# Kernel optimization log

Hardware: AMD Instinct MI355X
Metric: run time of the kernel (lower is better)

## Reference

```python
import jax, jax.numpy as jnp
import numpy as np

N = 100000   # nodes
E = 1600000  # edges
D = 128      # in_dim
H = 128      # hidden


def setup_inputs() -> dict:
    key = jax.random.key(0)
    k = jax.random.split(key, 6)
    x = jax.random.normal(k[0], (N, D), dtype=jnp.float32)
    edge_index = jax.random.randint(k[1], (2, E), 0, N, dtype=jnp.int64)
    s1 = 1.0 / np.sqrt(D)
    s2 = 1.0 / np.sqrt(H)
    W1 = jax.random.uniform(k[2], (D, H), jnp.float32, -s1, s1)
    b1 = jax.random.uniform(k[3], (H,), jnp.float32, -s1, s1)
    W2 = jax.random.uniform(k[4], (H, H), jnp.float32, -s2, s2)
    b2 = jax.random.uniform(k[5], (H,), jnp.float32, -s2, s2)
    return {"x": x, "W1": W1, "b1": b1, "W2": W2, "b2": b2,
            "edge_index": edge_index}


def reference(x, W1, b1, W2, b2, edge_index):
    n = x.shape[0]
    loop = jnp.arange(n, dtype=edge_index.dtype)
    src = jnp.concatenate([edge_index[0], loop])  # sources incl. self-loops
    dst = jnp.concatenate([edge_index[1], loop])  # targets incl. self-loops
    # symmetric GCN normalization: D^-1/2 A_hat D^-1/2
    deg = jax.ops.segment_sum(jnp.ones_like(dst, jnp.float32), dst,
                              num_segments=n)
    dinv = jnp.where(deg > 0, deg ** -0.5, 0.0)
    norm = dinv[src] * dinv[dst]  # [E+N]

    def gcn_conv(h, W, b):
        m = h @ W                                   # [N, H] transform first
        agg = jax.ops.segment_sum(norm[:, None] * m[src], dst,
                                  num_segments=n)   # gather-scale-scatter
        return agg + b

    h = jax.nn.relu(gcn_conv(x, W1, b1))  # dropout is identity in eval mode
    return gcn_conv(h, W2, b2)
```

## Files before the change

kernel.cpp:

```cpp
#include <hip/hip_runtime.h>


#define RB    9
#define RANGE 512
#define CAPB  16384
#define CHUNK 8192

typedef __attribute__((ext_vector_type(8))) short bf16x8;
typedef __attribute__((ext_vector_type(4))) float f32x4;

__device__ inline float bf_lo(unsigned w) { return __uint_as_float(w << 16); }
__device__ inline float bf_hi(unsigned w) { return __uint_as_float(w & 0xffff0000u); }
__device__ inline unsigned bf16pair(float lo, float hi) {
    unsigned a = __float_as_uint(lo), b = __float_as_uint(hi);
    a += 0x7fffu + ((a >> 16) & 1u);
    b += 0x7fffu + ((b >> 16) & 1u);
    return (a >> 16) | (b & 0xffff0000u);
}
__device__ inline unsigned short bf16rne(float f) {
    unsigned u = __float_as_uint(f);
    u += 0x7fffu + ((u >> 16) & 1u);
    return (unsigned short)(u >> 16);
}
__device__ inline float bf2f(unsigned short h) { return __uint_as_float(((unsigned)h) << 16); }

__global__ void detect_i64(const unsigned* ei, int E, int* flag) {
    __shared__ int nz;
    if (threadIdx.x == 0) nz = 0;
    __syncthreads();
    int samples = E < 2048 ? E : 2048;
    int cnt = 0;
    for (int i = threadIdx.x; i < samples; i += blockDim.x)
        if (ei[2 * i + 1] != 0u) cnt++;
    if (cnt) atomicAdd(&nz, cnt);
    __syncthreads();
    if (threadIdx.x == 0) *flag = (nz == 0) ? 1 : 0;
}

__global__ void init_gcur(unsigned* gcur, int NB) {
    int b = blockIdx.x * blockDim.x + threadIdx.x;
    if (b < NB) gcur[b] = (unsigned)b * CAPB;
}

__global__ __launch_bounds__(256) void bucketA(const unsigned* __restrict__ ei, int E, int n,
                                               const int* __restrict__ flag,
                                               unsigned* __restrict__ gcur,
                                               unsigned* __restrict__ recs) {
    __shared__ unsigned hist[512];
    __shared__ unsigned offs[512];
    const int t = threadIdx.x;
    const int NB = (n + RANGE - 1) >> RB;
    for (int i = t; i < NB; i += 256) hist[i] = 0u;
    __syncthreads();
    const int base = blockIdx.x * CHUNK;
    const bool i64 = (*flag != 0);
    unsigned rec[32], bk[32];
#pragma unroll
    for (int j = 0; j < 32; j++) {
        int i = base + j * 256 + t;
        unsigned bv = 0xffffffffu, rv = 0u;
        if (i < E) {
            unsigned s, d;
            if (i64) { s = ei[2 * (size_t)i]; d = ei[2 * ((size_t)E + i)]; }
            else     { s = ei[i];             d = ei[(size_t)E + i]; }
            bv = d >> RB;
            rv = (s << RB) | (d & (RANGE - 1));
            atomicAdd(&hist[bv], 1u);
        }
        rec[j] = rv; bk[j] = bv;
    }
    __syncthreads();
    for (int b = t; b < NB; b += 256) {
        unsigned h = hist[b];
        offs[b] = h ? atomicAdd(&gcur[b], h) : 0u;
    }
    __syncthreads();
#pragma unroll
    for (int j = 0; j < 32; j++) {
        unsigned b = bk[j];
        if (b != 0xffffffffu) {
            unsigned pos = atomicAdd(&offs[b], 1u);
            if (pos < (b + 1u) * CAPB) recs[pos] = rec[j];
        }
    }
}

__global__ __launch_bounds__(256) void bucket_deg(const unsigned* __restrict__ gcur,
                                                  const unsigned* __restrict__ recs,
                                                  unsigned* __restrict__ deg, int n) {
    __shared__ unsigned dl[RANGE];
    const int b = blockIdx.x, t = threadIdx.x;
    const int node0 = b << RB;
    for (int v = t; v < RANGE; v += 256) dl[v] = 1u;
    __syncthreads();
    unsigned base = (unsigned)b * CAPB;
    unsigned cnt = gcur[b] - base; if (cnt > CAPB) cnt = CAPB;
    for (unsigned i = t; i < cnt; i += 256)
        atomicAdd(&dl[recs[base + i] & (RANGE - 1)], 1u);
    __syncthreads();
    for (int v = t; v < RANGE; v += 256)
        if (node0 + v < n) deg[node0 + v] = dl[v];
}

__global__ void dinv_kernel(const unsigned* deg, float* dinv, int n) {
    int i = blockIdx.x * blockDim.x + threadIdx.x;
    if (i < n) dinv[i] = rsqrtf((float)deg[i]);
}

__global__ void scan_block_sums(const unsigned* deg, unsigned* partials, int n) {
    __shared__ unsigned sdata[256];
    int b = blockIdx.x, t = threadIdx.x;
    int base = b * 1024;
    unsigned s = 0;
    for (int j = 0; j < 4; j++) {
        int i = base + t * 4 + j;
        if (i < n) s += deg[i];
    }
    sdata[t] = s;
    __syncthreads();
    for (int stride = 128; stride > 0; stride >>= 1) {
        if (t < stride) sdata[t] += sdata[t + stride];
        __syncthreads();
    }
    if (t == 0) partials[b] = sdata[0];
}

__global__ void scan_partials(unsigned* partials, int nb) {
    if (threadIdx.x == 0 && blockIdx.x == 0) {
        unsigned run = 0;
        for (int i = 0; i < nb; i++) { unsigned v = partials[i]; partials[i] = run; run += v; }
    }
}

__global__ void scan_write(const unsigned* deg, const unsigned* partials,
                           int* row_off, int n) {
    int b = blockIdx.x, t = threadIdx.x;
    int lane = t & 63, wid = t >> 6;
    int base = b * 1024;
    unsigned vals[4];
    unsigned s = 0;
    for (int j = 0; j < 4; j++) {
        int i = base + t * 4 + j;
        vals[j] = (i < n) ? deg[i] : 0u;
        s += vals[j];
    }
    unsigned inc = s;
    for (int o = 1; o < 64; o <<= 1) {
        unsigned u = (unsigned)__shfl_up((int)inc, o, 64);
        if (lane >= o) inc += u;
    }
    __shared__ unsigned wtot[4];
    if (lane == 63) wtot[wid] = inc;
    __syncthreads();
    unsigned wbase = 0;
    for (int w = 0; w < wid; w++) wbase += wtot[w];
    unsigned excl = partials[b] + wbase + (inc - s);
    for (int j = 0; j < 4; j++) {
        int i = base + t * 4 + j;
        if (i < n) { row_off[i] = (int)excl; excl += vals[j]; }
    }
}

__global__ __launch_bounds__(256) void bucket_csr(const unsigned* __restrict__ gcur,
                                                  const unsigned* __restrict__ recs,
                                                  const int* __restrict__ row_off,
                                                  int* __restrict__ csr, int n) {
    __shared__ int cur[RANGE];
    const int b = blockIdx.x, t = threadIdx.x;
    const int node0 = b << RB;
    for (int v = t; v < RANGE; v += 256) {
        int node = node0 + v;
        if (node < n) {
            int ro = row_off[node];
            csr[ro] = node;
            cur[v] = ro + 1;
        }
    }
    __syncthreads();
    unsigned base = (unsigned)b * CAPB;
    unsigned cnt = gcur[b] - base; if (cnt > CAPB) cnt = CAPB;
    for (unsigned i = t; i < cnt; i += 256) {
        unsigned r = recs[base + i];
        int pos = atomicAdd(&cur[r & (RANGE - 1)], 1);
        csr[pos] = (int)(r >> RB);
    }
}

__global__ void pack_w(const float* __restrict__ W, uint4* __restrict__ Bhi,
                       uint4* __restrict__ Blo) {
    int idx = blockIdx.x * 256 + threadIdx.x;
    int lane = idx & 63, ks = (idx >> 6) & 3, nt = idx >> 8;
    int j = nt * 16 + (lane & 15);
    int k0 = ks * 32 + ((lane >> 4) & 3) * 8;
    unsigned hi[4], lo[4];
#pragma unroll
    for (int p = 0; p < 4; p++) {
        float w0 = W[(size_t)(k0 + 2 * p) * 128 + j];
        float w1 = W[(size_t)(k0 + 2 * p + 1) * 128 + j];
        unsigned short h0 = bf16rne(w0), h1 = bf16rne(w1);
        unsigned short l0 = bf16rne(w0 - bf2f(h0)), l1 = bf16rne(w1 - bf2f(h1));
        hi[p] = (unsigned)h0 | ((unsigned)h1 << 16);
        lo[p] = (unsigned)l0 | ((unsigned)l1 << 16);
    }
    Bhi[idx] = make_uint4(hi[0], hi[1], hi[2], hi[3]);
    Blo[idx] = make_uint4(lo[0], lo[1], lo[2], lo[3]);
}

template <int SPLIT>
__global__ __launch_bounds__(256) void gemm_mfma(const void* __restrict__ Ain,
                                                 const uint4* __restrict__ Bhi,
                                                 const uint4* __restrict__ Blo,
                                                 const float* __restrict__ dinv,
                                                 unsigned short* __restrict__ Mout, int M) {
    __shared__ unsigned short Ahi[64 * 128];
    __shared__ unsigned short Alo[SPLIT ? 64 * 128 : 64];
    const int t = threadIdx.x;
    const int row0 = blockIdx.x * 64;
    char* ah8 = (char*)Ahi;
    char* al8 = (char*)Alo;

    if (SPLIT) {
        const float4* A4 = (const float4*)Ain;
#pragma unroll
        for (int it = 0; it < 4; it++) {
            int i = it * 256 + t;
            int r = i >> 4, c8 = i & 15;
            int gr = row0 + r;
            float4 v0 = make_float4(0.f, 0.f, 0.f, 0.f), v1 = v0;
            if (gr < M) { v0 = A4[(size_t)gr * 32 + c8 * 2]; v1 = A4[(size_t)gr * 32 + c8 * 2 + 1]; }
            float f[8] = {v0.x, v0.y, v0.z, v0.w, v1.x, v1.y, v1.z, v1.w};
            unsigned hp[4], lp[4];
#pragma unroll
            for (int p = 0; p < 4; p++) {
                unsigned short h0 = bf16rne(f[2 * p]), h1 = bf16rne(f[2 * p + 1]);
                unsigned short l0 = bf16rne(f[2 * p] - bf2f(h0));
                unsigned short l1 = bf16rne(f[2 * p + 1] - bf2f(h1));
                hp[p] = (unsigned)h0 | ((unsigned)h1 << 16);
                lp[p] = (unsigned)l0 | ((unsigned)l1 << 16);
            }
            int byte = (r * 256 + c8 * 16) ^ ((r & 7) << 4);
            *(uint4*)(ah8 + byte) = make_uint4(hp[0], hp[1], hp[2], hp[3]);
            *(uint4*)(al8 + byte) = make_uint4(lp[0], lp[1], lp[2], lp[3]);
        }
    } else {
        const uint4* A4 = (const uint4*)Ain;
#pragma unroll
        for (int it = 0; it < 4; it++) {
            int i = it * 256 + t;
            int r = i >> 4, c8 = i & 15;
            int gr = row0 + r;
            uint4 v = make_uint4(0u, 0u, 0u, 0u);
            if (gr < M) v = A4[(size_t)gr * 16 + c8];
            int byte = (r * 256 + c8 * 16) ^ ((r & 7) << 4);
            *(uint4*)(ah8 + byte) = v;
        }
    }
    __syncthreads();

    const int wv = t >> 6, lane = t & 63;
    const int arow = wv * 16 + (lane & 15);
    const int kh = ((lane >> 4) & 3) * 8;
    f32x4 acc[8];
#pragma unroll
    for (int nt = 0; nt < 8; nt++) acc[nt] = (f32x4){0.f, 0.f, 0.f, 0.f};
    float dv[4];
    const int orow0 = row0 + wv * 16 + ((lane >> 4) & 3) * 4;
#pragma unroll
    for (int r = 0; r < 4; r++) {
        int rr = orow0 + r;
        dv[r] = (rr < M) ? dinv[rr] : 0.f;
    }
#pragma unroll
    for (int ks = 0; ks < 4; ks++) {
        int byte = (arow * 256 + (ks * 32 + kh) * 2) ^ ((arow & 7) << 4);
        bf16x8 a_h = *(const bf16x8*)(ah8 + byte);
        bf16x8 a_l;
        if (SPLIT) a_l = *(const bf16x8*)(al8 + byte);
#pragma unroll
        for (int nt = 0; nt < 8; nt++) {
            uint4 bhv = Bhi[(nt * 4 + ks) * 64 + lane];
            uint4 blv = Blo[(nt * 4 + ks) * 64 + lane];
            bf16x8 bh = *(bf16x8*)&bhv;
            bf16x8 bl = *(bf16x8*)&blv;
            acc[nt] = __builtin_amdgcn_mfma_f32_16x16x32_bf16(a_h, bh, acc[nt], 0, 0, 0);
            if (SPLIT) acc[nt] = __builtin_amdgcn_mfma_f32_16x16x32_bf16(a_l, bh, acc[nt], 0, 0, 0);
            acc[nt] = __builtin_amdgcn_mfma_f32_16x16x32_bf16(a_h, bl, acc[nt], 0, 0, 0);
        }
    }
    __syncthreads();
#pragma unroll
    for (int nt = 0; nt < 8; nt++) {
#pragma unroll
        for (int r = 0; r < 4; r++) {
            int lr = wv * 16 + ((lane >> 4) & 3) * 4 + r;
            int byte = (lr * 256 + (nt * 16 + (lane & 15)) * 2) ^ ((lr & 7) << 4);
            *(unsigned short*)(ah8 + byte) = bf16rne(acc[nt][r] * dv[r]);
        }
    }
    __syncthreads();
#pragma unroll
    for (int it = 0; it < 4; it++) {
        int i = it * 256 + t;
        int r = i >> 4, c8 = i & 15;
        int gr = row0 + r;
        if (gr < M) {
            int byte = (r * 256 + c8 * 16) ^ ((r & 7) << 4);
            *(uint4*)(Mout + (size_t)gr * 128 + c8 * 8) = *(uint4*)(ah8 + byte);
        }
    }
}

__global__ __launch_bounds__(256) void agg_kernel(const unsigned* __restrict__ m,
                                                  const int* __restrict__ csr,
                                                  const int* __restrict__ row_off,
                                                  const unsigned* __restrict__ deg,
                                                  const float* __restrict__ dinv,
                                                  const float* __restrict__ bias,
                                                  void* __restrict__ outp, int n, int mode) {
    int wid = threadIdx.x >> 6, lane = threadIdx.x & 63;
    int v = blockIdx.x * 4 + wid;
    if (v >= n) return;
    int start = row_off[v];
    int cnt = (int)deg[v];
    float ax = 0.f, ay = 0.f;
    int e = 0;
    while (e < cnt) {
        int nload = cnt - e;
        if (nload > 64) nload = 64;
        int sv = 0;
        if (lane < nload) sv = csr[start + e + lane];
        int j = 0;
        for (; j + 16 <= nload; j += 16) {
            unsigned w[16];
#pragma unroll
            for (int q = 0; q < 16; q++) {
                int s = __shfl(sv, j + q);
                w[q] = m[(size_t)s * 64 + lane];
            }
#pragma unroll
            for (int q = 0; q < 16; q++) { ax += bf_lo(w[q]); ay += bf_hi(w[q]); }
        }
        if (j + 8 <= nload) {
            unsigned w[8];
#pragma unroll
            for (int q = 0; q < 8; q++) {
                int s = __shfl(sv, j + q);
                w[q] = m[(size_t)s * 64 + lane];
            }
#pragma unroll
            for (int q = 0; q < 8; q++) { ax += bf_lo(w[q]); ay += bf_hi(w[q]); }
            j += 8;
        }
        for (; j < nload; j++) {
            int s = __shfl(sv, j);
            unsigned w = m[(size_t)s * 64 + lane];
            ax += bf_lo(w); ay += bf_hi(w);
        }
        e += nload;
    }
    float dv = dinv[v];
    float2 b = ((const float2*)bias)[lane];
    float ox = fmaf(dv, ax, b.x), oy = fmaf(dv, ay, b.y);
    if (mode) {
        ox = fmaxf(ox, 0.f); oy = fmaxf(oy, 0.f);
        ((unsigned*)outp)[(size_t)v * 64 + lane] = bf16pair(ox, oy);
    } else {
        ((float2*)outp)[(size_t)v * 64 + lane] = make_float2(ox, oy);
    }
}

extern "C" void kernel_launch(void* const* d_in, const int* in_sizes, int n_in,
                              void* d_out, int out_size, void* d_ws, size_t ws_size,
                              hipStream_t stream) {
    const float*    x  = (const float*)d_in[0];
    const float*    W1 = (const float*)d_in[1];
    const float*    b1 = (const float*)d_in[2];
    const float*    W2 = (const float*)d_in[3];
    const float*    b2 = (const float*)d_in[4];
    const unsigned* ei = (const unsigned*)d_in[5];
    int n = in_sizes[0] / 128;
    int E = in_sizes[5] / 2;
    float* out = (float*)d_out;
    int NB = (n + RANGE - 1) >> RB;

    char* w = (char*)d_ws;
    size_t off = 0;
    auto alloc = [&](size_t bytes) -> void* {
        void* p = w + off;
        off = (off + bytes + 255) & ~(size_t)255;
        return p;
    };
    int*            flag     = (int*)alloc(4);
    unsigned*       deg      = (unsigned*)alloc((size_t)n * 4);
    float*          dinv     = (float*)alloc((size_t)n * 4);
    int*            row_off  = (int*)alloc((size_t)n * 4);
    unsigned*       partials = (unsigned*)alloc(4096 * 4);
    unsigned*       gcur     = (unsigned*)alloc(512 * 4);
    uint4*          Bhi1     = (uint4*)alloc(2048 * 16);
    uint4*          Blo1     = (uint4*)alloc(2048 * 16);
    uint4*          Bhi2     = (uint4*)alloc(2048 * 16);
    uint4*          Blo2     = (uint4*)alloc(2048 * 16);
    unsigned*       recs     = (unsigned*)alloc((size_t)NB * CAPB * 4);
    int*            csr      = (int*)alloc((size_t)(E + n) * 4);
    unsigned short* m_bf     = (unsigned short*)alloc((size_t)n * 128 * 2);
    unsigned*       h_bf     = (unsigned*)alloc((size_t)n * 64 * 4);
    (void)ws_size; (void)n_in; (void)out_size;

    int nb = (n + 1023) / 1024;
    int nchunk = (E + CHUNK - 1) / CHUNK;

    hipLaunchKernelGGL(detect_i64, dim3(1), dim3(256), 0, stream, ei, E, flag);
    hipLaunchKernelGGL(init_gcur, dim3((NB + 255) / 256), dim3(256), 0, stream, gcur, NB);
    hipLaunchKernelGGL(pack_w, dim3(8), dim3(256), 0, stream, W1, Bhi1, Blo1);
    hipLaunchKernelGGL(pack_w, dim3(8), dim3(256), 0, stream, W2, Bhi2, Blo2);
    hipLaunchKernelGGL(bucketA, dim3(nchunk), dim3(256), 0, stream, ei, E, n, flag, gcur, recs);
    hipLaunchKernelGGL(bucket_deg, dim3(NB), dim3(256), 0, stream, gcur, recs, deg, n);
    hipLaunchKernelGGL(dinv_kernel, dim3((n + 255) / 256), dim3(256), 0, stream, deg, dinv, n);
    hipLaunchKernelGGL(scan_block_sums, dim3(nb), dim3(256), 0, stream, deg, partials, n);
    hipLaunchKernelGGL(scan_partials, dim3(1), dim3(64), 0, stream, partials, nb);
    hipLaunchKernelGGL(scan_write, dim3(nb), dim3(256), 0, stream, deg, partials, row_off, n);
    hipLaunchKernelGGL(bucket_csr, dim3(NB), dim3(256), 0, stream, gcur, recs, row_off, csr, n);

    int gblocks = (n + 63) / 64;
    hipLaunchKernelGGL((gemm_mfma<1>), dim3(gblocks), dim3(256), 0, stream,
                       (const void*)x, Bhi1, Blo1, dinv, m_bf, n);
    hipLaunchKernelGGL(agg_kernel, dim3((n + 3) / 4), dim3(256), 0, stream,
                       (const unsigned*)m_bf, csr, row_off, deg, dinv, b1, (void*)h_bf, n, 1);
    hipLaunchKernelGGL((gemm_mfma<0>), dim3(gblocks), dim3(256), 0, stream,
                       (const void*)h_bf, Bhi2, Blo2, dinv, m_bf, n);
    hipLaunchKernelGGL(agg_kernel, dim3((n + 3) / 4), dim3(256), 0, stream,
                       (const unsigned*)m_bf, csr, row_off, deg, dinv, b2, (void*)out, n, 0);
}
```

Measured before the change: 262.0 us.

## Store features in column-sliced layout and aggregate per slice for cache locality

The GEMM now writes the bf16 message matrix as 8 column slices of 16 features each ([slice][node][16]) instead of row-major 128-wide rows. The second GEMM reads the hidden activations in the same sliced layout. A new aggregation kernel assigns each block to one slice, so the random gathers for that slice touch a 3.2 MB working set that may stay in L2/MALL, and each 8-lane group handles one node. It also folds the dinv computation into bucket_deg, removing one launch. The risk is more total blocks and divergence within each 8-node wave, since the loop runs to the largest degree among those nodes, plus 32-byte gathers that underuse cache lines.

```diff
diff --git a/kernel.cpp b/kernel.cpp
--- a/kernel.cpp
+++ b/kernel.cpp
@@ -87,7 +87,8 @@
 
 __global__ __launch_bounds__(256) void bucket_deg(const unsigned* __restrict__ gcur,
                                                   const unsigned* __restrict__ recs,
-                                                  unsigned* __restrict__ deg, int n) {
+                                                  unsigned* __restrict__ deg,
+                                                  float* __restrict__ dinv, int n) {
     __shared__ unsigned dl[RANGE];
     const int b = blockIdx.x, t = threadIdx.x;
     const int node0 = b << RB;
@@ -99,12 +100,10 @@
         atomicAdd(&dl[recs[base + i] & (RANGE - 1)], 1u);
     __syncthreads();
     for (int v = t; v < RANGE; v += 256)
-        if (node0 + v < n) deg[node0 + v] = dl[v];
-}
-
-__global__ void dinv_kernel(const unsigned* deg, float* dinv, int n) {
-    int i = blockIdx.x * blockDim.x + threadIdx.x;
-    if (i < n) dinv[i] = rsqrtf((float)deg[i]);
+        if (node0 + v < n) {
+            deg[node0 + v] = dl[v];
+            dinv[node0 + v] = rsqrtf((float)dl[v]);
+        }
 }
 
 __global__ void scan_block_sums(const unsigned* deg, unsigned* partials, int n) {
@@ -243,15 +242,15 @@
             *(uint4*)(al8 + byte) = make_uint4(lp[0], lp[1], lp[2], lp[3]);
         }
     } else {
-        const uint4* A4 = (const uint4*)Ain;
+        const unsigned short* A = (const unsigned short*)Ain;
 #pragma unroll
         for (int it = 0; it < 4; it++) {
             int i = it * 256 + t;
-            int r = i >> 4, c8 = i & 15;
+            int half = i & 1, r = (i >> 1) & 63, sl = i >> 7;
             int gr = row0 + r;
             uint4 v = make_uint4(0u, 0u, 0u, 0u);
-            if (gr < M) v = A4[(size_t)gr * 16 + c8];
-            int byte = (r * 256 + c8 * 16) ^ ((r & 7) << 4);
+            if (gr < M) v = *(const uint4*)(A + ((size_t)sl * M + gr) * 16 + half * 8);
+            int byte = (r * 256 + sl * 32 + half * 16) ^ ((r & 7) << 4);
             *(uint4*)(ah8 + byte) = v;
         }
     }
@@ -301,71 +300,58 @@
 #pragma unroll
     for (int it = 0; it < 4; it++) {
         int i = it * 256 + t;
-        int r = i >> 4, c8 = i & 15;
+        int half = i & 1, r = (i >> 1) & 63, sl = i >> 7;
         int gr = row0 + r;
         if (gr < M) {
-            int byte = (r * 256 + c8 * 16) ^ ((r & 7) << 4);
-            *(uint4*)(Mout + (size_t)gr * 128 + c8 * 8) = *(uint4*)(ah8 + byte);
-        }
-    }
-}
-
-__global__ __launch_bounds__(256) void agg_kernel(const unsigned* __restrict__ m,
-                                                  const int* __restrict__ csr,
-                                                  const int* __restrict__ row_off,
-                                                  const unsigned* __restrict__ deg,
-                                                  const float* __restrict__ dinv,
-                                                  const float* __restrict__ bias,
-                                                  void* __restrict__ outp, int n, int mode) {
-    int wid = threadIdx.x >> 6, lane = threadIdx.x & 63;
-    int v = blockIdx.x * 4 + wid;
-    if (v >= n) return;
-    int start = row_off[v];
-    int cnt = (int)deg[v];
+            int byte = (r * 256 + sl * 32 + half * 16) ^ ((r & 7) << 4);
+            *(uint4*)(Mout + ((size_t)sl * M + gr) * 16 + half * 8) = *(uint4*)(ah8 + byte);
+        }
+    }
+}
+
+__global__ __launch_bounds__(256) void agg_slice(const unsigned* __restrict__ mm,
+                                                 const int* __restrict__ csr,
+                                                 const int* __restrict__ row_off,
+                                                 const unsigned* __restrict__ deg,
+                                                 const float* __restrict__ dinv,
+                                                 const float* __restrict__ bias,
+                                                 void* __restrict__ outp, int n, int mode) {
+    const int s = blockIdx.x & 7;
+    const int chunk = blockIdx.x >> 3;
+    const int wid = threadIdx.x >> 6, lane = threadIdx.x & 63;
+    const int g = lane >> 3, j = lane & 7;
+    const unsigned* ms = mm + (size_t)s * n * 8;
+    const int v = chunk * 32 + wid * 8 + g;
+
+    int cnt = 0, start = 0;
+    if (v < n) { cnt = (int)deg[v]; start = row_off[v]; }
+    int mc = cnt;
+    mc = max(mc, __shfl_xor(mc, 8));
+    mc = max(mc, __shfl_xor(mc, 16));
+    mc = max(mc, __shfl_xor(mc, 32));
+
     float ax = 0.f, ay = 0.f;
-    int e = 0;
-    while (e < cnt) {
-        int nload = cnt - e;
-        if (nload > 64) nload = 64;
+    for (int e0 = 0; e0 < mc; e0 += 8) {
         int sv = 0;
-        if (lane < nload) sv = csr[start + e + lane];
-        int j = 0;
-        for (; j + 16 <= nload; j += 16) {
-            unsigned w[16];
-#pragma unroll
-            for (int q = 0; q < 16; q++) {
-                int s = __shfl(sv, j + q);
-                w[q] = m[(size_t)s * 64 + lane];
-            }
-#pragma unroll
-            for (int q = 0; q < 16; q++) { ax += bf_lo(w[q]); ay += bf_hi(w[q]); }
-        }
-        if (j + 8 <= nload) {
-            unsigned w[8];
-#pragma unroll
-            for (int q = 0; q < 8; q++) {
-                int s = __shfl(sv, j + q);
-                w[q] = m[(size_t)s * 64 + lane];
-            }
-#pragma unroll
-            for (int q = 0; q < 8; q++) { ax += bf_lo(w[q]); ay += bf_hi(w[q]); }
-            j += 8;
-        }
-        for (; j < nload; j++) {
-            int s = __shfl(sv, j);
-            unsigned w = m[(size_t)s * 64 + lane];
+        if (e0 + j < cnt) sv = csr[start + e0 + j];
+#pragma unroll
+        for (int sub = 0; sub < 8; sub++) {
+            int src = __shfl(sv, g * 8 + sub);
+            unsigned w = 0u;
+            if (e0 + sub < cnt) w = ms[(size_t)src * 8 + j];
             ax += bf_lo(w); ay += bf_hi(w);
         }
-        e += nload;
-    }
-    float dv = dinv[v];
-    float2 b = ((const float2*)bias)[lane];
-    float ox = fmaf(dv, ax, b.x), oy = fmaf(dv, ay, b.y);
-    if (mode) {
-        ox = fmaxf(ox, 0.f); oy = fmaxf(oy, 0.f);
-        ((unsigned*)outp)[(size_t)v * 64 + lane] = bf16pair(ox, oy);
-    } else {
-        ((float2*)outp)[(size_t)v * 64 + lane] = make_float2(ox, oy);
+    }
+    if (v < n) {
+        float dv = dinv[v];
+        float bx = bias[s * 16 + 2 * j], by = bias[s * 16 + 2 * j + 1];
+        float ox = fmaf(dv, ax, bx), oy = fmaf(dv, ay, by);
+        if (mode) {
+            ox = fmaxf(ox, 0.f); oy = fmaxf(oy, 0.f);
+            ((unsigned*)outp)[((size_t)s * n + v) * 8 + j] = bf16pair(ox, oy);
+        } else {
+            ((float2*)outp)[(size_t)v * 64 + s * 8 + j] = make_float2(ox, oy);
+        }
     }
 }
 
@@ -414,20 +400,20 @@
     hipLaunchKernelGGL(pack_w, dim3(8), dim3(256), 0, stream, W1, Bhi1, Blo1);
     hipLaunchKernelGGL(pack_w, dim3(8), dim3(256), 0, stream, W2, Bhi2, Blo2);
     hipLaunchKernelGGL(bucketA, dim3(nchunk), dim3(256), 0, stream, ei, E, n, flag, gcur, recs);
-    hipLaunchKernelGGL(bucket_deg, dim3(NB), dim3(256), 0, stream, gcur, recs, deg, n);
-    hipLaunchKernelGGL(dinv_kernel, dim3((n + 255) / 256), dim3(256), 0, stream, deg, dinv, n);
+    hipLaunchKernelGGL(bucket_deg, dim3(NB), dim3(256), 0, stream, gcur, recs, deg, dinv, n);
     hipLaunchKernelGGL(scan_block_sums, dim3(nb), dim3(256), 0, stream, deg, partials, n);
     hipLaunchKernelGGL(scan_partials, dim3(1), dim3(64), 0, stream, partials, nb);
     hipLaunchKernelGGL(scan_write, dim3(nb), dim3(256), 0, stream, deg, partials, row_off, n);
     hipLaunchKernelGGL(bucket_csr, dim3(NB), dim3(256), 0, stream, gcur, recs, row_off, csr, n);
 
     int gblocks = (n + 63) / 64;
+    int ablocks = 8 * ((n + 31) / 32);
     hipLaunchKernelGGL((gemm_mfma<1>), dim3(gblocks), dim3(256), 0, stream,
                        (const void*)x, Bhi1, Blo1, dinv, m_bf, n);
-    hipLaunchKernelGGL(agg_kernel, dim3((n + 3) / 4), dim3(256), 0, stream,
+    hipLaunchKernelGGL(agg_slice, dim3(ablocks), dim3(256), 0, stream,
                        (const unsigned*)m_bf, csr, row_off, deg, dinv, b1, (void*)h_bf, n, 1);
     hipLaunchKernelGGL((gemm_mfma<0>), dim3(gblocks), dim3(256), 0, stream,
                        (const void*)h_bf, Bhi2, Blo2, dinv, m_bf, n);
-    hipLaunchKernelGGL(agg_kernel, dim3((n + 3) / 4), dim3(256), 0, stream,
+    hipLaunchKernelGGL(agg_slice, dim3(ablocks), dim3(256), 0, stream,
                        (const unsigned*)m_bf, csr, row_off, deg, dinv, b2, (void*)out, n, 0);
 }
```

Measured after the change: 284.1 us. 8.4% more time.
